# Performance work log

Measured on AMD Instinct MI355X. Metric: run time of the kernel, lower is better.

Reference implementation:

```python
import jax, jax.numpy as jnp
import numpy as np

ITEM_NUM = 50000
TARGET_ITEM_NUM = 50000
EMB = 128
N_LAYERS = 3
N_EDGES = 800000
N_NODES = ITEM_NUM + 1  # forward uses item_emb[:item_num+1]


def gcn_conv(x, row, col, W, b, n):
    """PyG GCNConv: symmetric-normalized aggregation with self-loops.
    out = D^{-1/2} (A + I) D^{-1/2} (x @ W) + b
    """
    h = x @ W  # [n, d]
    loops = jnp.arange(n)
    r = jnp.concatenate([row, loops])  # source
    c = jnp.concatenate([col, loops])  # target
    deg = jax.ops.segment_sum(jnp.ones(r.shape[0], x.dtype), c, num_segments=n)
    dinv = jnp.where(deg > 0, deg ** -0.5, jnp.zeros_like(deg))
    norm = dinv[r] * dinv[c]  # [E+n]
    out = jax.ops.segment_sum(h[r] * norm[:, None], c, num_segments=n)
    return out + b


def setup_inputs() -> dict:
    key = jax.random.key(0)
    k0, k1, k2 = jax.random.split(key, 3)
    edge_index = jax.random.randint(k0, (2, N_EDGES), 0, N_NODES)
    total = ITEM_NUM + TARGET_ITEM_NUM + 1
    # xavier_uniform for embedding table and per-layer GCN weights
    lim_e = float(np.sqrt(6.0 / (total + EMB)))
    item_emb = jax.random.uniform(k1, (total, EMB), jnp.float32, -lim_e, lim_e)
    lim_w = float(np.sqrt(6.0 / (EMB + EMB)))
    W = jax.random.uniform(k2, (N_LAYERS, EMB, EMB), jnp.float32, -lim_w, lim_w)
    b = jnp.zeros((N_LAYERS, EMB), jnp.float32)
    return {"edge_index": edge_index, "item_emb": item_emb, "W": W, "b": b}


def reference(edge_index, item_emb, W, b):
    n = N_NODES
    row, col = edge_index[0], edge_index[1]
    embeds = [item_emb[:n]]
    for i in range(N_LAYERS):
        embeds.append(gcn_conv(embeds[-1], row, col, W[i], b[i], n))
    return sum(embeds)  # [n, EMB], sum over layer embeddings
```

## Files before the change

### kernel.cpp

```cpp
#include <hip/hip_runtime.h>
#include <hip/hip_bf16.h>


constexpr int NN   = 50001;
constexpr int D    = 128;
constexpr int NPAD = 50048;
constexpr int NBK  = 196;
constexpr int CAP  = 7680;
constexpr int ZROW = NPAD - 1;

using bf16x8 = __attribute__((ext_vector_type(8))) short;
using f32x4  = __attribute__((ext_vector_type(4))) float;
using f32x2  = __attribute__((ext_vector_type(2))) float;
using u16x8  = __attribute__((ext_vector_type(8))) unsigned short;
using u32x4  = __attribute__((ext_vector_type(4))) unsigned;

__device__ __forceinline__ ushort f2b(float f) {
    unsigned u = __float_as_uint(f);
    return (ushort)((u + 0x7FFFu + ((u >> 16) & 1u)) >> 16);
}
__device__ __forceinline__ float b2f(ushort u) {
    return __uint_as_float((unsigned)u << 16);
}

__global__ __launch_bounds__(256)
void k_build(const int* __restrict__ row, const int* __restrict__ col,
             int* __restrict__ partCur, unsigned* __restrict__ part,
             const float* __restrict__ W, ushort* __restrict__ Wt,
             const float* __restrict__ emb, ushort* __restrict__ xb, int E, int n) {
    int b = blockIdx.x, t = threadIdx.x;
    if (b < NBK) {
        __shared__ int hist[256];
        __shared__ int base[256];
        hist[t] = 0;
        __syncthreads();
        int e0 = b * 4096;
        unsigned rec[16];
        int bkt[16];
#pragma unroll
        for (int k = 0; k < 16; k++) {
            int e = e0 + k * 256 + t;
            if (e < E) {
                int r = row[e], c = col[e];
                rec[k] = (unsigned)r | ((unsigned)(c & 255) << 16);
                bkt[k] = c >> 8;
                atomicAdd(&hist[bkt[k]], 1);
            } else bkt[k] = -1;
        }
        __syncthreads();
        if (hist[t] > 0) base[t] = t * CAP + atomicAdd(&partCur[t], hist[t]);
        __syncthreads();
#pragma unroll
        for (int k = 0; k < 16; k++) {
            if (bkt[k] >= 0) {
                int pos = atomicAdd(&base[bkt[k]], 1);
                if (pos < (bkt[k] + 1) * CAP) part[pos] = rec[k];
            }
        }
    } else if (b < NBK + 192) {
        int idx = (b - NBK) * 256 + t;
        int l = idx >> 14, rem = idx & 16383;
        int c = rem >> 7, k = rem & 127;
        Wt[idx] = f2b(W[l * D * D + k * D + c]);
    } else {
        int i4 = (b - NBK - 192) * 256 + t;
        if (i4 >= NPAD * (D / 4)) return;
        int r = i4 >> 5;
        if (r < n) {
            float4 v = ((const float4*)emb)[i4];
            ushort4 o; o.x = f2b(v.x); o.y = f2b(v.y); o.z = f2b(v.z); o.w = f2b(v.w);
            ((ushort4*)xb)[i4] = o;
        } else {
            ((ushort4*)xb)[i4] = make_ushort4(0, 0, 0, 0);
        }
    }
}

__global__ __launch_bounds__(256)
void k_scat(const unsigned* __restrict__ part, const int* __restrict__ partCur,
            float* __restrict__ dinv, unsigned* __restrict__ rp,
            ushort* __restrict__ meta, int n) {
    __shared__ int hist[256];
    __shared__ int sm[256];
    __shared__ int off[256];
    __shared__ int cur[256];
    int b = blockIdx.x, t = threadIdx.x;
    int node0 = b * 256;
    int nn = min(256, n - node0);
    int T = min(partCur[b], CAP);
    const unsigned* pb = part + (size_t)b * CAP;
    hist[t] = 0;
    __syncthreads();
    for (int i = t; i < T; i += 256) atomicAdd(&hist[pb[i] >> 16], 1);
    __syncthreads();
    int v = hist[t];
    int pv = (v + 15) & ~15;
    sm[t] = pv;
    __syncthreads();
    for (int ofs = 1; ofs < 256; ofs <<= 1) {
        int u = (t >= ofs) ? sm[t - ofs] : 0;
        __syncthreads();
        sm[t] += u;
        __syncthreads();
    }
    off[t] = sm[t] - pv;
    cur[t] = 0;
    if (t < nn) {
        dinv[node0 + t] = rsqrtf((float)v + 1.0f);
        rp[node0 + t] = (unsigned)(b * CAP + off[t]) | ((unsigned)v << 21);
    }
    __syncthreads();
    for (int i = t; i < T; i += 256) {
        unsigned rec = pb[i];
        int dl = (int)(rec >> 16);
        int pos = off[dl] + atomicAdd(&cur[dl], 1);
        if (pos < CAP) meta[(size_t)b * CAP + pos] = (ushort)(rec & 0xFFFFu);
    }
    int base = off[t];
    for (int p = v; p < pv; p++)
        if (base + p < CAP) meta[(size_t)b * CAP + base + p] = (ushort)ZROW;
}

constexpr int WT_LD = 136;
__global__ __launch_bounds__(256)
void k_gemm_mfma(const ushort* __restrict__ xb, const ushort* __restrict__ WtL,
                 const float* __restrict__ dinv, ushort* __restrict__ h, int n) {
    __shared__ ushort wlds[D * WT_LD];
    for (int idx = threadIdx.x; idx < D * (D / 8); idx += 256) {
        int r = idx >> 4, c8 = (idx & 15) * 8;
        *(uint4*)&wlds[r * WT_LD + c8] = *(const uint4*)&WtL[r * D + c8];
    }
    __syncthreads();

    int wave = threadIdx.x >> 6, lane = threadIdx.x & 63;
    int q = lane >> 4, i = lane & 15;
    int waveRow = blockIdx.x * 128 + wave * 32;

    bf16x8 a[2][4];
#pragma unroll
    for (int rt = 0; rt < 2; rt++) {
        const ushort* base = &xb[(size_t)(waveRow + rt * 16 + i) * D + q * 8];
#pragma unroll
        for (int ks = 0; ks < 4; ks++)
            a[rt][ks] = *(const bf16x8*)(base + ks * 32);
    }

    f32x4 acc[2][8] = {};
#pragma unroll
    for (int ct = 0; ct < 8; ct++) {
        const ushort* wbase = &wlds[(ct * 16 + i) * WT_LD + q * 8];
#pragma unroll
        for (int ks = 0; ks < 4; ks++) {
            bf16x8 bfr = *(const bf16x8*)(wbase + ks * 32);
            acc[0][ct] = __builtin_amdgcn_mfma_f32_16x16x32_bf16(a[0][ks], bfr, acc[0][ct], 0, 0, 0);
            acc[1][ct] = __builtin_amdgcn_mfma_f32_16x16x32_bf16(a[1][ks], bfr, acc[1][ct], 0, 0, 0);
        }
    }

#pragma unroll
    for (int rt = 0; rt < 2; rt++)
#pragma unroll
        for (int r4 = 0; r4 < 4; r4++) {
            int row = waveRow + rt * 16 + q * 4 + r4;
            float dv = (row < n) ? dinv[row] : 0.f;
#pragma unroll
            for (int ct = 0; ct < 8; ct++)
                h[(size_t)ct * (NPAD * 16) + (size_t)row * 16 + i] =
                    f2b(acc[rt][ct][r4] * dv);
        }
}

__global__ __launch_bounds__(256)
void k_pull(const unsigned* __restrict__ rp, const ushort* __restrict__ meta,
            const ushort* __restrict__ h,
            const float* __restrict__ dinv, const float* __restrict__ bias,
            ushort* __restrict__ xb_out,
            const float* __restrict__ emb, const ushort* __restrict__ x1,
            const ushort* __restrict__ x2, float* __restrict__ out,
            int n, int mode) {
    int slice = blockIdx.x & 7;
    int node  = (blockIdx.x >> 3) * 128 + (threadIdx.x >> 1);
    int l     = threadIdx.x & 1;
    int f0    = slice * 16 + l * 8;
    size_t o  = (size_t)node * D + f0;
    if (node >= n) {
        if (mode == 0) {
            u16x8 z = {0, 0, 0, 0, 0, 0, 0, 0};
            *(u16x8*)(xb_out + o) = z;
        }
        return;
    }
    const ushort* hs = h + (size_t)slice * (NPAD * 16) + l * 8;

    unsigned pk = rp[node];
    int s   = (int)(pk & 0x1FFFFFu);
    int deg = (int)(pk >> 21);

    u32x4 sv = *(const u32x4*)(hs + (size_t)node * 16);
    float di = dinv[node];
    const float4* bp = (const float4*)(bias + f0);
    float4 b0 = bp[0], b1 = bp[1];
    float4 e0, e1; u16x8 w1, w2;
    if (mode) {
        const float4* ep = (const float4*)(emb + o);
        e0 = ep[0]; e1 = ep[1];
        w1 = *(const u16x8*)(x1 + o);
        w2 = *(const u16x8*)(x2 + o);
    }

    float accL[4], accH[4];
#pragma unroll
    for (int k = 0; k < 4; k++) {
        accL[k] = __uint_as_float(sv[k] << 16);
        accH[k] = __uint_as_float(sv[k] & 0xFFFF0000u);
    }

    for (int j = 0; j < deg; j += 16) {
        u16x8 m0 = *(const u16x8*)&meta[s + j];
        u16x8 m1 = *(const u16x8*)&meta[s + j + 8];
        u32x4 v[16];
#pragma unroll
        for (int u = 0; u < 8; u++) v[u]     = *(const u32x4*)(hs + (size_t)m0[u] * 16);
#pragma unroll
        for (int u = 0; u < 8; u++) v[8 + u] = *(const u32x4*)(hs + (size_t)m1[u] * 16);
#pragma unroll
        for (int u = 0; u < 16; u++)
#pragma unroll
            for (int k = 0; k < 4; k++) {
                accL[k] += __uint_as_float(v[u][k] << 16);
                accH[k] += __uint_as_float(v[u][k] & 0xFFFF0000u);
            }
    }

    float r0 = fmaf(accL[0], di, b0.x);
    float r1 = fmaf(accH[0], di, b0.y);
    float r2 = fmaf(accL[1], di, b0.z);
    float r3 = fmaf(accH[1], di, b0.w);
    float r4 = fmaf(accL[2], di, b1.x);
    float r5 = fmaf(accH[2], di, b1.y);
    float r6 = fmaf(accL[3], di, b1.z);
    float r7 = fmaf(accH[3], di, b1.w);
    if (mode == 0) {
        u16x8 w;
        w[0] = f2b(r0); w[1] = f2b(r1); w[2] = f2b(r2); w[3] = f2b(r3);
        w[4] = f2b(r4); w[5] = f2b(r5); w[6] = f2b(r6); w[7] = f2b(r7);
        *(u16x8*)(xb_out + o) = w;
    } else {
        f32x4 o0, o1;
        o0[0] = e0.x + b2f(w1[0]) + b2f(w2[0]) + r0;
        o0[1] = e0.y + b2f(w1[1]) + b2f(w2[1]) + r1;
        o0[2] = e0.z + b2f(w1[2]) + b2f(w2[2]) + r2;
        o0[3] = e0.w + b2f(w1[3]) + b2f(w2[3]) + r3;
        o1[0] = e1.x + b2f(w1[4]) + b2f(w2[4]) + r4;
        o1[1] = e1.y + b2f(w1[5]) + b2f(w2[5]) + r5;
        o1[2] = e1.z + b2f(w1[6]) + b2f(w2[6]) + r6;
        o1[3] = e1.w + b2f(w1[7]) + b2f(w2[7]) + r7;
        __builtin_nontemporal_store(o0, (f32x4*)(out + o));
        __builtin_nontemporal_store(o1, (f32x4*)(out + o) + 1);
    }
}

extern "C" void kernel_launch(void* const* d_in, const int* in_sizes, int n_in,
                              void* d_out, int out_size, void* d_ws, size_t ws_size,
                              hipStream_t stream) {
    const int*   edge = (const int*)d_in[0];
    const float* emb  = (const float*)d_in[1];
    const float* W    = (const float*)d_in[2];
    const float* b    = (const float*)d_in[3];
    float* out = (float*)d_out;

    const int E = in_sizes[0] / 2;
    const int n = NN;
    const int* row = edge;
    const int* col = edge + E;

    char* ws = (char*)d_ws;
    size_t off = 0;
    auto carve = [&](size_t bytes) { char* p = ws + off; off = (off + bytes + 511) / 512 * 512; return p; };
    int*      partCur = (int*)     carve(256 * 4);
    unsigned* part    = (unsigned*)carve((size_t)NBK * CAP * 4);
    ushort*   meta    = (ushort*)  carve((size_t)NBK * CAP * 2);
    unsigned* rp      = (unsigned*)carve((size_t)n * 4);
    float*    dinv    = (float*)   carve((size_t)n * 4);
    ushort*   Wt      = (ushort*)  carve((size_t)3 * D * D * 2);
    ushort*   xb0     = (ushort*)  carve((size_t)NPAD * D * 2);
    ushort*   xb1     = (ushort*)  carve((size_t)NPAD * D * 2);
    ushort*   xb2     = (ushort*)  carve((size_t)NPAD * D * 2);
    ushort*   h       = (ushort*)  carve((size_t)NPAD * D * 2);

    (void)hipMemsetAsync(partCur, 0, 256 * 4, stream);

    const int init_blocks  = (NPAD * (D / 4) + 255) / 256;
    const int build_blocks = NBK + 192 + init_blocks;
    k_build<<<build_blocks, 256, 0, stream>>>(row, col, partCur, part, W, Wt, emb, xb0, E, n);
    k_scat <<<NBK, 256, 0, stream>>>(part, partCur, dinv, rp, meta, n);

    const int gemm_blocks = NPAD / 128;
    const int pull_blocks = (NPAD / 128) * 8;
    ushort* xin[3]  = {xb0, xb1, xb2};
    ushort* xout[3] = {xb1, xb2, nullptr};
    for (int l = 0; l < 3; l++) {
        k_gemm_mfma<<<gemm_blocks, 256, 0, stream>>>(xin[l], Wt + (size_t)l * D * D, dinv, h, n);
        k_pull<<<pull_blocks, 256, 0, stream>>>(rp, meta, h,
                                                dinv, b + (size_t)l * D, xout[l],
                                                emb, xb1, xb2, out, n, (l < 2) ? 0 : 1);
    }
}
```

Measured before the change: 275.5 us.

## Pin feature slices to XCDs with persistent work-queue pull kernel

The pull kernel becomes persistent with 2048 blocks. Each block reads its XCC ID and first works on the feature slice matching that XCD, taking 128-node chunks from a per-slice atomic counter before moving on to other slices. The aim is to keep each slice's gather traffic inside one XCD's L2 and to balance work dynamically across blocks. It adds an atomic and two barriers per chunk, plus a larger memset to zero the counters, and it depends on how blocks are distributed across XCDs.

```diff
diff --git a/kernel.cpp b/kernel.cpp
--- a/kernel.cpp
+++ b/kernel.cpp
@@ -2,12 +2,13 @@
 #include <hip/hip_bf16.h>
 
 
-constexpr int NN   = 50001;
-constexpr int D    = 128;
-constexpr int NPAD = 50048;
-constexpr int NBK  = 196;
-constexpr int CAP  = 7680;
-constexpr int ZROW = NPAD - 1;
+constexpr int NN     = 50001;
+constexpr int D      = 128;
+constexpr int NPAD   = 50048;
+constexpr int NBK    = 196;
+constexpr int CAP    = 7680;
+constexpr int ZROW   = NPAD - 1;
+constexpr int NCHUNK = NPAD / 128;
 
 using bf16x8 = __attribute__((ext_vector_type(8))) short;
 using f32x4  = __attribute__((ext_vector_type(4))) float;
@@ -165,7 +166,7 @@
             float dv = (row < n) ? dinv[row] : 0.f;
 #pragma unroll
             for (int ct = 0; ct < 8; ct++)
-                h[(size_t)ct * (NPAD * 16) + (size_t)row * 16 + i] =
+                h[(size_t)ct * ((size_t)NPAD * 16) + (size_t)row * 16 + i] =
                     f2b(acc[rt][ct][r4] * dv);
         }
 }
@@ -177,86 +178,102 @@
             ushort* __restrict__ xb_out,
             const float* __restrict__ emb, const ushort* __restrict__ x1,
             const ushort* __restrict__ x2, float* __restrict__ out,
-            int n, int mode) {
-    int slice = blockIdx.x & 7;
-    int node  = (blockIdx.x >> 3) * 128 + (threadIdx.x >> 1);
-    int l     = threadIdx.x & 1;
-    int f0    = slice * 16 + l * 8;
-    size_t o  = (size_t)node * D + f0;
-    if (node >= n) {
-        if (mode == 0) {
-            u16x8 z = {0, 0, 0, 0, 0, 0, 0, 0};
-            *(u16x8*)(xb_out + o) = z;
-        }
-        return;
-    }
-    const ushort* hs = h + (size_t)slice * (NPAD * 16) + l * 8;
-
-    unsigned pk = rp[node];
-    int s   = (int)(pk & 0x1FFFFFu);
-    int deg = (int)(pk >> 21);
-
-    u32x4 sv = *(const u32x4*)(hs + (size_t)node * 16);
-    float di = dinv[node];
-    const float4* bp = (const float4*)(bias + f0);
-    float4 b0 = bp[0], b1 = bp[1];
-    float4 e0, e1; u16x8 w1, w2;
-    if (mode) {
-        const float4* ep = (const float4*)(emb + o);
-        e0 = ep[0]; e1 = ep[1];
-        w1 = *(const u16x8*)(x1 + o);
-        w2 = *(const u16x8*)(x2 + o);
-    }
-
-    float accL[4], accH[4];
-#pragma unroll
-    for (int k = 0; k < 4; k++) {
-        accL[k] = __uint_as_float(sv[k] << 16);
-        accH[k] = __uint_as_float(sv[k] & 0xFFFF0000u);
-    }
-
-    for (int j = 0; j < deg; j += 16) {
-        u16x8 m0 = *(const u16x8*)&meta[s + j];
-        u16x8 m1 = *(const u16x8*)&meta[s + j + 8];
-        u32x4 v[16];
-#pragma unroll
-        for (int u = 0; u < 8; u++) v[u]     = *(const u32x4*)(hs + (size_t)m0[u] * 16);
-#pragma unroll
-        for (int u = 0; u < 8; u++) v[8 + u] = *(const u32x4*)(hs + (size_t)m1[u] * 16);
-#pragma unroll
-        for (int u = 0; u < 16; u++)
+            int* __restrict__ wq, int n, int mode) {
+    int xcc;
+    asm volatile("s_getreg_b32 %0, hwreg(HW_REG_XCC_ID)" : "=s"(xcc));
+    int myslice = xcc & 7;
+    int tid = threadIdx.x;
+    int l   = tid & 1;
+    __shared__ int sh_chunk;
+
+    for (int so = 0; so < 8; so++) {
+        int slice = (myslice + so) & 7;
+        int f0 = slice * 16 + l * 8;
+        const ushort* hs = h + (size_t)slice * ((size_t)NPAD * 16) + l * 8;
+        const float4* bp = (const float4*)(bias + f0);
+        float4 b0 = bp[0], b1 = bp[1];
+
+        for (;;) {
+            __syncthreads();
+            if (tid == 0) sh_chunk = atomicAdd(wq + slice, 1);
+            __syncthreads();
+            int c = sh_chunk;
+            if (c >= NCHUNK) break;
+
+            int node = c * 128 + (tid >> 1);
+            size_t o = (size_t)node * D + f0;
+            if (node >= n) {
+                if (mode == 0) {
+                    u16x8 z = {0, 0, 0, 0, 0, 0, 0, 0};
+                    *(u16x8*)(xb_out + o) = z;
+                }
+                continue;
+            }
+            unsigned pk = rp[node];
+            int s   = (int)(pk & 0x1FFFFFu);
+            int deg = (int)(pk >> 21);
+
+            u32x4 sv = *(const u32x4*)(hs + (size_t)node * 16);
+            float di = dinv[node];
+            float4 e0, e1; u16x8 w1, w2;
+            if (mode) {
+                const float4* ep = (const float4*)(emb + o);
+                e0 = ep[0]; e1 = ep[1];
+                w1 = *(const u16x8*)(x1 + o);
+                w2 = *(const u16x8*)(x2 + o);
+            }
+
+            float accL[4], accH[4];
 #pragma unroll
             for (int k = 0; k < 4; k++) {
-                accL[k] += __uint_as_float(v[u][k] << 16);
-                accH[k] += __uint_as_float(v[u][k] & 0xFFFF0000u);
-            }
-    }
-
-    float r0 = fmaf(accL[0], di, b0.x);
-    float r1 = fmaf(accH[0], di, b0.y);
-    float r2 = fmaf(accL[1], di, b0.z);
-    float r3 = fmaf(accH[1], di, b0.w);
-    float r4 = fmaf(accL[2], di, b1.x);
-    float r5 = fmaf(accH[2], di, b1.y);
-    float r6 = fmaf(accL[3], di, b1.z);
-    float r7 = fmaf(accH[3], di, b1.w);
-    if (mode == 0) {
-        u16x8 w;
-        w[0] = f2b(r0); w[1] = f2b(r1); w[2] = f2b(r2); w[3] = f2b(r3);
-        w[4] = f2b(r4); w[5] = f2b(r5); w[6] = f2b(r6); w[7] = f2b(r7);
-        *(u16x8*)(xb_out + o) = w;
-    } else {
-        f32x4 o0, o1;
-        o0[0] = e0.x + b2f(w1[0]) + b2f(w2[0]) + r0;
-        o0[1] = e0.y + b2f(w1[1]) + b2f(w2[1]) + r1;
-        o0[2] = e0.z + b2f(w1[2]) + b2f(w2[2]) + r2;
-        o0[3] = e0.w + b2f(w1[3]) + b2f(w2[3]) + r3;
-        o1[0] = e1.x + b2f(w1[4]) + b2f(w2[4]) + r4;
-        o1[1] = e1.y + b2f(w1[5]) + b2f(w2[5]) + r5;
-        o1[2] = e1.z + b2f(w1[6]) + b2f(w2[6]) + r6;
-        o1[3] = e1.w + b2f(w1[7]) + b2f(w2[7]) + r7;
-        __builtin_nontemporal_store(o0, (f32x4*)(out + o));
-        __builtin_nontemporal_store(o1, (f32x4*)(out + o) + 1);
+                accL[k] = __uint_as_float(sv[k] << 16);
+                accH[k] = __uint_as_float(sv[k] & 0xFFFF0000u);
+            }
+
+            for (int j = 0; j < deg; j += 16) {
+                u16x8 m0 = *(const u16x8*)&meta[s + j];
+                u16x8 m1 = *(const u16x8*)&meta[s + j + 8];
+                u32x4 v[16];
+#pragma unroll
+                for (int u = 0; u < 8; u++) v[u]     = *(const u32x4*)(hs + (size_t)m0[u] * 16);
+#pragma unroll
+                for (int u = 0; u < 8; u++) v[8 + u] = *(const u32x4*)(hs + (size_t)m1[u] * 16);
+#pragma unroll
+                for (int u = 0; u < 16; u++)
+#pragma unroll
+                    for (int k = 0; k < 4; k++) {
+                        accL[k] += __uint_as_float(v[u][k] << 16);
+                        accH[k] += __uint_as_float(v[u][k] & 0xFFFF0000u);
+                    }
+            }
+
+            float r0 = fmaf(accL[0], di, b0.x);
+            float r1 = fmaf(accH[0], di, b0.y);
+            float r2 = fmaf(accL[1], di, b0.z);
+            float r3 = fmaf(accH[1], di, b0.w);
+            float r4 = fmaf(accL[2], di, b1.x);
+            float r5 = fmaf(accH[2], di, b1.y);
+            float r6 = fmaf(accL[3], di, b1.z);
+            float r7 = fmaf(accH[3], di, b1.w);
+            if (mode == 0) {
+                u16x8 w;
+                w[0] = f2b(r0); w[1] = f2b(r1); w[2] = f2b(r2); w[3] = f2b(r3);
+                w[4] = f2b(r4); w[5] = f2b(r5); w[6] = f2b(r6); w[7] = f2b(r7);
+                *(u16x8*)(xb_out + o) = w;
+            } else {
+                f32x4 o0, o1;
+                o0[0] = e0.x + b2f(w1[0]) + b2f(w2[0]) + r0;
+                o0[1] = e0.y + b2f(w1[1]) + b2f(w2[1]) + r1;
+                o0[2] = e0.z + b2f(w1[2]) + b2f(w2[2]) + r2;
+                o0[3] = e0.w + b2f(w1[3]) + b2f(w2[3]) + r3;
+                o1[0] = e1.x + b2f(w1[4]) + b2f(w2[4]) + r4;
+                o1[1] = e1.y + b2f(w1[5]) + b2f(w2[5]) + r5;
+                o1[2] = e1.z + b2f(w1[6]) + b2f(w2[6]) + r6;
+                o1[3] = e1.w + b2f(w1[7]) + b2f(w2[7]) + r7;
+                __builtin_nontemporal_store(o0, (f32x4*)(out + o));
+                __builtin_nontemporal_store(o1, (f32x4*)(out + o) + 1);
+            }
+        }
     }
 }
 
@@ -278,6 +295,7 @@
     size_t off = 0;
     auto carve = [&](size_t bytes) { char* p = ws + off; off = (off + bytes + 511) / 512 * 512; return p; };
     int*      partCur = (int*)     carve(256 * 4);
+    int*      workCtr = (int*)     carve(3 * 8 * 4);
     unsigned* part    = (unsigned*)carve((size_t)NBK * CAP * 4);
     ushort*   meta    = (ushort*)  carve((size_t)NBK * CAP * 2);
     unsigned* rp      = (unsigned*)carve((size_t)n * 4);
@@ -288,7 +306,7 @@
     ushort*   xb2     = (ushort*)  carve((size_t)NPAD * D * 2);
     ushort*   h       = (ushort*)  carve((size_t)NPAD * D * 2);
 
-    (void)hipMemsetAsync(partCur, 0, 256 * 4, stream);
+    (void)hipMemsetAsync(partCur, 0, 1024 + 512, stream);
 
     const int init_blocks  = (NPAD * (D / 4) + 255) / 256;
     const int build_blocks = NBK + 192 + init_blocks;
@@ -296,13 +314,14 @@
     k_scat <<<NBK, 256, 0, stream>>>(part, partCur, dinv, rp, meta, n);
 
     const int gemm_blocks = NPAD / 128;
-    const int pull_blocks = (NPAD / 128) * 8;
+    const int pull_blocks = 2048;
     ushort* xin[3]  = {xb0, xb1, xb2};
     ushort* xout[3] = {xb1, xb2, nullptr};
     for (int l = 0; l < 3; l++) {
         k_gemm_mfma<<<gemm_blocks, 256, 0, stream>>>(xin[l], Wt + (size_t)l * D * D, dinv, h, n);
         k_pull<<<pull_blocks, 256, 0, stream>>>(rp, meta, h,
                                                 dinv, b + (size_t)l * D, xout[l],
-                                                emb, xb1, xb2, out, n, (l < 2) ? 0 : 1);
-    }
-}
+                                                emb, xb1, xb2, out,
+                                                workCtr + l * 8, n, (l < 2) ? 0 : 1);
+    }
+}
```

Result: slower. 869.3 us (+215.5%).
